# Optimization experiments

Hardware: AMD Instinct MI355X
Metric: run time of the kernel (lower is better)

The kernel has to match this reference:

```python
import jax, jax.numpy as jnp
import numpy as np

B, S, H, E, K, NH = 2, 2048, 1024, 8, 2, 8
HD = H // NH          # head dim = 128
HQ = H // 4           # seasonal encoder width = 256
CAP = int(B * S * 1.5 * K / E)  # expert capacity = 1536


def setup_inputs() -> dict:
    key = jax.random.key(0)
    ks = iter(jax.random.split(key, 32))

    def lin(shape):
        fan_in = shape[0]
        return jax.random.normal(next(ks), shape, jnp.float32) / np.sqrt(fan_in)

    inp = {
        "hidden_states": jax.random.normal(next(ks), (B, S, H), jnp.float32),
        # position embedding table [sequence_length, H]
        "pos_emb": jax.random.normal(next(ks), (S, H), jnp.float32) * 0.02,
        # temporal_encoder: Linear(H+2,H) -> ReLU -> Linear(H,H)
        "We1": lin((H + 2, H)), "be1": jnp.zeros((H,), jnp.float32),
        "We2": lin((H, H)),     "be2": jnp.zeros((H,), jnp.float32),
        # seasonal_encoder: Linear(1,H//4) -> ReLU -> Linear(H//4,H//4)
        "Ws1": lin((1, HQ)),   "bs1": jnp.zeros((HQ,), jnp.float32),
        "Ws2": lin((HQ, HQ)),  "bs2": jnp.zeros((HQ,), jnp.float32),
        # temporal_attention (MultiheadAttention, 8 heads)
        "Wq": lin((H, H)), "bq": jnp.zeros((H,), jnp.float32),
        "Wk": lin((H, H)), "bk": jnp.zeros((H,), jnp.float32),
        "Wv": lin((H, H)), "bv": jnp.zeros((H,), jnp.float32),
        "Wo": lin((H, H)), "bo": jnp.zeros((H,), jnp.float32),
        # temporal_router: Linear(H,H) -> ReLU -> Linear(H,E)
        "Wr1": lin((H, H)), "br1": jnp.zeros((H,), jnp.float32),
        "Wr2": lin((H, E)), "br2": jnp.zeros((E,), jnp.float32),
    }
    return inp


def _forward(hidden_states, pos_emb, We1, be1, We2, be2, Ws1, bs1, Ws2, bs2,
             Wq, bq, Wk, bk, Wv, bv, Wo, bo, Wr1, br1, Wr2, br2):
    b, s, h = hidden_states.shape
    # time features (time_info is None -> defaults)
    t = jnp.arange(s, dtype=jnp.float32)                   # [S]
    season = jnp.sin(t * 2.0 * jnp.pi / 24.0)              # [S]
    time_feat = jnp.broadcast_to(jnp.stack([t, season], -1), (b, s, 2))

    combined = jnp.concatenate([hidden_states, time_feat], axis=-1)  # [B,S,H+2]
    enc = jax.nn.relu(combined @ We1 + be1) @ We2 + be2              # [B,S,H]

    pos = pos_emb[:s]                                                # [S,H]
    seas = jax.nn.relu(season[:, None] @ Ws1 + bs1) @ Ws2 + bs2      # [S,H//4]
    seas_full = jnp.tile(seas, (1, h // seas.shape[-1]))             # [S,H] (expand to H)

    x = enc + pos[None] + seas_full[None]                            # [B,S,H]

    # self-attention (eval mode, no dropout)
    def heads(y):
        return y.reshape(b, s, NH, HD)
    q = heads(x @ Wq + bq)
    k = heads(x @ Wk + bk)
    v = heads(x @ Wv + bv)
    scores = jnp.einsum('bqhd,bkhd->bhqk', q, k) / np.sqrt(HD)
    attn = jax.nn.softmax(scores, axis=-1)
    ctx = jnp.einsum('bhqk,bkhd->bqhd', attn, v).reshape(b, s, h)
    x = ctx @ Wo + bo

    logits = jax.nn.relu(x @ Wr1 + br1) @ Wr2 + br2                  # [B,S,E]
    probs = jax.nn.softmax(logits, axis=-1)

    topv, topi = jax.lax.top_k(probs, K)                             # [B,S,K]
    topv = topv / topv.sum(-1, keepdims=True)

    onehot = jax.nn.one_hot(topi, E, dtype=probs.dtype)              # [B,S,K,E]
    disp0 = onehot.sum(-2)                                           # [B,S,E] (0/1)
    comb0 = (topv[..., None] * onehot).sum(-2)                       # [B,S,E]

    # only capacity slot 0 is ever written (per original code)
    dispatch = jnp.zeros((b, s, E, CAP), probs.dtype).at[..., 0].set(disp0)
    combine = jnp.zeros((b, s, E, CAP), probs.dtype).at[..., 0].set(comb0)

    p_mean = probs.mean(axis=(0, 1))                                 # [E]
    aux_loss = jnp.sum(p_mean * jnp.log(p_mean * E + 1e-9))
    return dispatch, combine, probs, aux_loss


def reference(hidden_states, pos_emb, We1, be1, We2, be2, Ws1, bs1, Ws2, bs2,
              Wq, bq, Wk, bk, Wv, bv, Wo, bo, Wr1, br1, Wr2, br2):
    return _forward(hidden_states, pos_emb, We1, be1, We2, be2, Ws1, bs1, Ws2, bs2,
                    Wq, bq, Wk, bk, Wv, bv, Wo, bo, Wr1, br1, Wr2, br2)
```

## Files before the change

### kernel.cpp

```cpp
#include <hip/hip_runtime.h>
#include <hip/hip_fp16.h>
#include <math.h>

#define N_TOK 4096
#define S_LEN 2048
#define H_DIM 1024
#define E_EXP 8
#define CAPV  1536
#define NHEAD 8
#define HDHD  128

typedef __attribute__((ext_vector_type(8))) _Float16 v8h;
typedef __attribute__((ext_vector_type(4))) float v4f;

__device__ __forceinline__ void splitf16(float v, unsigned short& h, unsigned short& l) {
    __half hh = __float2half(v);
    h = __half_as_ushort(hh);
    l = __half_as_ushort(__float2half(v - __half2float(hh)));
}

__device__ __forceinline__ void gld_lds16(const void* g, void* l) {
    __builtin_amdgcn_global_load_lds(
        (const __attribute__((address_space(1))) unsigned int*)g,
        (__attribute__((address_space(3))) unsigned int*)l,
        16, 0, 0);
}

__global__ __launch_bounds__(256) void prep_k(
    const float* __restrict__ hid, unsigned short* __restrict__ hi,
    unsigned short* __restrict__ lo,
    const float* __restrict__ Ws1, const float* __restrict__ bs1,
    const float* __restrict__ Ws2, const float* __restrict__ bs2,
    float* __restrict__ seasons, float* __restrict__ seas24,
    const float* __restrict__ Wr2, float* __restrict__ wr2t) {
    __shared__ float hbuf[256];
    int blk = blockIdx.x;
    int tid = threadIdx.x;
    if (blk < 4096) {
        int i = blk * 256 + tid;
        float4 v = ((const float4*)hid)[i];
        ushort4 h, l;
        splitf16(v.x, h.x, l.x);
        splitf16(v.y, h.y, l.y);
        splitf16(v.z, h.z, l.z);
        splitf16(v.w, h.w, l.w);
        ((ushort4*)hi)[i] = h;
        ((ushort4*)lo)[i] = l;
    } else if (blk < 4104) {
        int s = (blk - 4096) * 256 + tid;
        if (s < S_LEN) {
            double a = (double)s * 2.0 * M_PI / 24.0;
            seasons[s] = (float)sin(a);
        }
    } else if (blk < 4128) {
        int m = blk - 4104;
        double a = (double)m * 2.0 * M_PI / 24.0;
        float sv = (float)sin(a);
        int j = tid;
        hbuf[j] = fmaxf(sv * Ws1[j] + bs1[j], 0.f);
        __syncthreads();
        float acc = bs2[j];
        for (int i = 0; i < 256; ++i) acc = fmaf(hbuf[i], Ws2[i * 256 + j], acc);
        seas24[m * 256 + j] = acc;
    } else {
        int i = (blk - 4128) * 256 + tid;
        int k = i >> 3, e = i & 7;
        wr2t[e * 1024 + k] = Wr2[i];
    }
}

__device__ __forceinline__ void wconv_body(const float* __restrict__ W,
                                           unsigned short* __restrict__ Thi,
                                           unsigned short* __restrict__ Tlo) {
    __shared__ unsigned short Hs[64][65];
    __shared__ unsigned short Ls[64][65];
    int k0 = blockIdx.y * 64, n0 = blockIdx.x * 64;
    int tid = threadIdx.x;
#pragma unroll
    for (int i = 0; i < 4; ++i) {
        int idx = tid + i * 256;
        int kk = idx >> 4, n4 = idx & 15;
        float4 v = *(const float4*)(W + (size_t)(k0 + kk) * 1024 + n0 + n4 * 4);
        unsigned short h, l;
        splitf16(v.x, h, l); Hs[n4 * 4 + 0][kk] = h; Ls[n4 * 4 + 0][kk] = l;
        splitf16(v.y, h, l); Hs[n4 * 4 + 1][kk] = h; Ls[n4 * 4 + 1][kk] = l;
        splitf16(v.z, h, l); Hs[n4 * 4 + 2][kk] = h; Ls[n4 * 4 + 2][kk] = l;
        splitf16(v.w, h, l); Hs[n4 * 4 + 3][kk] = h; Ls[n4 * 4 + 3][kk] = l;
    }
    __syncthreads();
#pragma unroll
    for (int i = 0; i < 4; ++i) {
        int idx = tid + i * 256;
        int n = idx >> 4, k4 = idx & 15;
        ushort4 h = make_ushort4(Hs[n][k4 * 4], Hs[n][k4 * 4 + 1], Hs[n][k4 * 4 + 2], Hs[n][k4 * 4 + 3]);
        ushort4 l = make_ushort4(Ls[n][k4 * 4], Ls[n][k4 * 4 + 1], Ls[n][k4 * 4 + 2], Ls[n][k4 * 4 + 3]);
        *(ushort4*)(Thi + (size_t)(n0 + n) * 1024 + k0 + k4 * 4) = h;
        *(ushort4*)(Tlo + (size_t)(n0 + n) * 1024 + k0 + k4 * 4) = l;
    }
}

struct WBatch {
    const float* src[7];
    unsigned short* dh[7];
    unsigned short* dl[7];
};

__global__ __launch_bounds__(256) void wconv_batch_k(WBatch wb) {
    int i = blockIdx.z;
    wconv_body(wb.src[i], wb.dh[i], wb.dl[i]);
}

template <int MODE, int EMITF, int EMITS, int EMITT>
__global__ __launch_bounds__(256, 2) void gemm_split(
    const unsigned short* __restrict__ Ahi, const unsigned short* __restrict__ Alo,
    const unsigned short* __restrict__ WThi, const unsigned short* __restrict__ WTlo,
    const float* __restrict__ bias, float* __restrict__ Cf,
    unsigned short* __restrict__ Chi, unsigned short* __restrict__ Clo,
    const float* __restrict__ rowT, const float* __restrict__ rowS,
    const float* __restrict__ seasons, const float* __restrict__ pos,
    const float* __restrict__ seas24, float escale) {
    __shared__ unsigned short Ash[2][128 * 32];
    __shared__ unsigned short Asl[2][128 * 32];
    __shared__ unsigned short Bsh[2][64 * 32];
    __shared__ unsigned short Bsl[2][64 * 32];
    int tid = threadIdx.x;
    int lane = tid & 63, w = tid >> 6;
    int l15 = lane & 15, l16 = lane >> 4;
    int wm = (w >> 1) * 64, wn = (w & 1) * 32;

    int bid = blockIdx.x;
    int mp = (bid & 7) + ((bid >> 7) << 3);
    int np = (bid >> 3) & 15;
    int m0 = mp * 128, n0 = np * 64;

    int ac0 = w * 128 + lane;
    int ac1 = ac0 + 64;
    int bc  = w * 64 + lane;
    int ar0 = ac0 >> 2, ar1 = ac1 >> 2, bn = bc >> 2;
    size_t a_src0 = (size_t)(m0 + ar0) * 1024 + (((ac0 & 3) ^ (ar0 & 3)) * 8);
    size_t a_src1 = (size_t)(m0 + ar1) * 1024 + (((ac1 & 3) ^ (ar1 & 3)) * 8);
    size_t b_src  = (size_t)(n0 + bn) * 1024 + (((bc & 3) ^ (bn & 3)) * 8);

    int a_off[4], b_off[2];
#pragma unroll
    for (int mi = 0; mi < 4; ++mi) {
        int row = wm + mi * 16 + l15;
        a_off[mi] = row * 32 + ((l16 ^ (row & 3)) * 8);
    }
#pragma unroll
    for (int ni = 0; ni < 2; ++ni) {
        int n = wn + ni * 16 + l15;
        b_off[ni] = n * 32 + ((l16 ^ (n & 3)) * 8);
    }

    auto STAGE = [&](int buf, int k0) {
        gld_lds16(Ahi + a_src0 + k0, &Ash[buf][ac0 * 8]);
        gld_lds16(Ahi + a_src1 + k0, &Ash[buf][ac1 * 8]);
        gld_lds16(Alo + a_src0 + k0, &Asl[buf][ac0 * 8]);
        gld_lds16(Alo + a_src1 + k0, &Asl[buf][ac1 * 8]);
        gld_lds16(WThi + b_src + k0, &Bsh[buf][bc * 8]);
        gld_lds16(WTlo + b_src + k0, &Bsl[buf][bc * 8]);
    };

    v4f acc[4][2] = {};
    STAGE(0, 0);
    __syncthreads();

    for (int kk = 0; kk < 32; ++kk) {
        int cur = kk & 1;
        if (kk < 31) STAGE(cur ^ 1, (kk + 1) * 32);
        v8h ah[4], al[4], bh[2], bl[2];
#pragma unroll
        for (int mi = 0; mi < 4; ++mi) {
            ah[mi] = *(const v8h*)&Ash[cur][a_off[mi]];
            al[mi] = *(const v8h*)&Asl[cur][a_off[mi]];
        }
#pragma unroll
        for (int ni = 0; ni < 2; ++ni) {
            bh[ni] = *(const v8h*)&Bsh[cur][b_off[ni]];
            bl[ni] = *(const v8h*)&Bsl[cur][b_off[ni]];
        }
#pragma unroll
        for (int mi = 0; mi < 4; ++mi)
#pragma unroll
            for (int ni = 0; ni < 2; ++ni) {
                acc[mi][ni] = __builtin_amdgcn_mfma_f32_16x16x32_f16(ah[mi], bh[ni], acc[mi][ni], 0, 0, 0);
                acc[mi][ni] = __builtin_amdgcn_mfma_f32_16x16x32_f16(al[mi], bh[ni], acc[mi][ni], 0, 0, 0);
                acc[mi][ni] = __builtin_amdgcn_mfma_f32_16x16x32_f16(ah[mi], bl[ni], acc[mi][ni], 0, 0, 0);
            }
        __syncthreads();
    }

    if (EMITT) {
#pragma unroll
        for (int mi = 0; mi < 4; ++mi) {
            int row0 = m0 + wm + mi * 16 + l16 * 4;
            int bb = row0 >> 11, ss = row0 & 2047;
#pragma unroll
            for (int ni = 0; ni < 2; ++ni) {
                int col = n0 + wn + ni * 16 + l15;
                int hh = col >> 7, dd = col & 127;
                size_t base = ((size_t)((bb * 8 + hh) * 128 + dd)) * 2048 + ss;
                ushort4 vh, vl;
                float v0 = acc[mi][ni][0] + bias[col];
                float v1 = acc[mi][ni][1] + bias[col];
                float v2 = acc[mi][ni][2] + bias[col];
                float v3 = acc[mi][ni][3] + bias[col];
                splitf16(v0, vh.x, vl.x);
                splitf16(v1, vh.y, vl.y);
                splitf16(v2, vh.z, vl.z);
                splitf16(v3, vh.w, vl.w);
                *(ushort4*)(Chi + base) = vh;
                *(ushort4*)(Clo + base) = vl;
            }
        }
    } else {
#pragma unroll
        for (int mi = 0; mi < 4; ++mi) {
#pragma unroll
            for (int r = 0; r < 4; ++r) {
                int row = m0 + wm + mi * 16 + l16 * 4 + r;
                int s = row & (S_LEN - 1);
                float tval = 0.f, seval = 0.f;
                if (MODE == 1) { tval = (float)s; seval = seasons[s]; }
#pragma unroll
                for (int ni = 0; ni < 2; ++ni) {
                    int col = n0 + wn + ni * 16 + l15;
                    float v = acc[mi][ni][r] + bias[col];
                    if (MODE == 1) v += tval * rowT[col] + seval * rowS[col];
                    if (MODE == 2) v += pos[(size_t)s * 1024 + col] + seas24[(s % 24) * 256 + (col & 255)];
                    if (MODE == 1 || MODE == 3) v = fmaxf(v, 0.f);
                    size_t o = (size_t)row * 1024 + col;
                    if (EMITF) Cf[o] = v;
                    if (EMITS) {
                        unsigned short hu, lu;
                        splitf16(v * escale, hu, lu);
                        Chi[o] = hu; Clo[o] = lu;
                    }
                }
            }
        }
    }
}

__global__ __launch_bounds__(256, 2) void gemm_qkv(
    const unsigned short* __restrict__ Ahi, const unsigned short* __restrict__ Alo,
    const unsigned short* __restrict__ WT3hi, const unsigned short* __restrict__ WT3lo,
    const float* __restrict__ bq, const float* __restrict__ bk,
    const float* __restrict__ bv,
    unsigned short* __restrict__ Qhi, unsigned short* __restrict__ Qlo,
    unsigned short* __restrict__ Khi, unsigned short* __restrict__ Klo,
    unsigned short* __restrict__ VThi, unsigned short* __restrict__ VTlo,
    float qscale) {
    __shared__ unsigned short Ash[2][128 * 32];
    __shared__ unsigned short Asl[2][128 * 32];
    __shared__ unsigned short Bsh[2][64 * 32];
    __shared__ unsigned short Bsl[2][64 * 32];
    int tid = threadIdx.x;
    int lane = tid & 63, w = tid >> 6;
    int l15 = lane & 15, l16 = lane >> 4;
    int wm = (w >> 1) * 64, wn = (w & 1) * 32;

    int bid = blockIdx.x;
    int t = bid >> 3;
    int mp = (bid & 7) + (t / 48) * 8;
    int np = t % 48;
    int m0 = mp * 128;
    int wn0 = np * 64;

    int ac0 = w * 128 + lane;
    int ac1 = ac0 + 64;
    int bc  = w * 64 + lane;
    int ar0 = ac0 >> 2, ar1 = ac1 >> 2, bn = bc >> 2;
    size_t a_src0 = (size_t)(m0 + ar0) * 1024 + (((ac0 & 3) ^ (ar0 & 3)) * 8);
    size_t a_src1 = (size_t)(m0 + ar1) * 1024 + (((ac1 & 3) ^ (ar1 & 3)) * 8);
    size_t b_src  = (size_t)(wn0 + bn) * 1024 + (((bc & 3) ^ (bn & 3)) * 8);

    int a_off[4], b_off[2];
#pragma unroll
    for (int mi = 0; mi < 4; ++mi) {
        int row = wm + mi * 16 + l15;
        a_off[mi] = row * 32 + ((l16 ^ (row & 3)) * 8);
    }
#pragma unroll
    for (int ni = 0; ni < 2; ++ni) {
        int n = wn + ni * 16 + l15;
        b_off[ni] = n * 32 + ((l16 ^ (n & 3)) * 8);
    }

    auto STAGE = [&](int buf, int k0) {
        gld_lds16(Ahi + a_src0 + k0, &Ash[buf][ac0 * 8]);
        gld_lds16(Ahi + a_src1 + k0, &Ash[buf][ac1 * 8]);
        gld_lds16(Alo + a_src0 + k0, &Asl[buf][ac0 * 8]);
        gld_lds16(Alo + a_src1 + k0, &Asl[buf][ac1 * 8]);
        gld_lds16(WT3hi + b_src + k0, &Bsh[buf][bc * 8]);
        gld_lds16(WT3lo + b_src + k0, &Bsl[buf][bc * 8]);
    };

    v4f acc[4][2] = {};
    STAGE(0, 0);
    __syncthreads();

    for (int kk = 0; kk < 32; ++kk) {
        int cur = kk & 1;
        if (kk < 31) STAGE(cur ^ 1, (kk + 1) * 32);
        v8h ah[4], al[4], bh[2], bl[2];
#pragma unroll
        for (int mi = 0; mi < 4; ++mi) {
            ah[mi] = *(const v8h*)&Ash[cur][a_off[mi]];
            al[mi] = *(const v8h*)&Asl[cur][a_off[mi]];
        }
#pragma unroll
        for (int ni = 0; ni < 2; ++ni) {
            bh[ni] = *(const v8h*)&Bsh[cur][b_off[ni]];
            bl[ni] = *(const v8h*)&Bsl[cur][b_off[ni]];
        }
#pragma unroll
        for (int mi = 0; mi < 4; ++mi)
#pragma unroll
            for (int ni = 0; ni < 2; ++ni) {
                acc[mi][ni] = __builtin_amdgcn_mfma_f32_16x16x32_f16(ah[mi], bh[ni], acc[mi][ni], 0, 0, 0);
                acc[mi][ni] = __builtin_amdgcn_mfma_f32_16x16x32_f16(al[mi], bh[ni], acc[mi][ni], 0, 0, 0);
                acc[mi][ni] = __builtin_amdgcn_mfma_f32_16x16x32_f16(ah[mi], bl[ni], acc[mi][ni], 0, 0, 0);
            }
        __syncthreads();
    }

    if (np >= 32) {
        const float* bias = bv;
        int n0 = (np - 32) * 64;
#pragma unroll
        for (int mi = 0; mi < 4; ++mi) {
            int row0 = m0 + wm + mi * 16 + l16 * 4;
            int bb = row0 >> 11, ss = row0 & 2047;
#pragma unroll
            for (int ni = 0; ni < 2; ++ni) {
                int col = n0 + wn + ni * 16 + l15;
                int hh = col >> 7, dd = col & 127;
                size_t base = ((size_t)((bb * 8 + hh) * 128 + dd)) * 2048 + ss;
                ushort4 vh, vl;
                float v0 = acc[mi][ni][0] + bias[col];
                float v1 = acc[mi][ni][1] + bias[col];
                float v2 = acc[mi][ni][2] + bias[col];
                float v3 = acc[mi][ni][3] + bias[col];
                splitf16(v0, vh.x, vl.x);
                splitf16(v1, vh.y, vl.y);
                splitf16(v2, vh.z, vl.z);
                splitf16(v3, vh.w, vl.w);
                *(ushort4*)(VThi + base) = vh;
                *(ushort4*)(VTlo + base) = vl;
            }
        }
    } else {
        const float* bias = np < 16 ? bq : bk;
        unsigned short* Dhi = np < 16 ? Qhi : Khi;
        unsigned short* Dlo = np < 16 ? Qlo : Klo;
        float esc = np < 16 ? qscale : 1.f;
        int n0 = (np & 15) * 64;
#pragma unroll
        for (int mi = 0; mi < 4; ++mi) {
#pragma unroll
            for (int r = 0; r < 4; ++r) {
                int row = m0 + wm + mi * 16 + l16 * 4 + r;
#pragma unroll
                for (int ni = 0; ni < 2; ++ni) {
                    int col = n0 + wn + ni * 16 + l15;
                    float v = (acc[mi][ni][r] + bias[col]) * esc;
                    size_t o = (size_t)row * 1024 + col;
                    unsigned short hu, lu;
                    splitf16(v, hu, lu);
                    Dhi[o] = hu; Dlo[o] = lu;
                }
            }
        }
    }
}

__global__ __launch_bounds__(256, 4) void attn_mfma_k(
    const unsigned short* __restrict__ qhi, const unsigned short* __restrict__ qlo,
    const unsigned short* __restrict__ khi, const unsigned short* __restrict__ klo,
    const unsigned short* __restrict__ vthi, const unsigned short* __restrict__ vtlo,
    float* __restrict__ OP, float* __restrict__ ML) {
    __shared__ unsigned short Ks_hi[32 * 128];
    __shared__ unsigned short Ks_lo[32 * 128];
    __shared__ unsigned short Vs_hi[128 * 32];
    __shared__ unsigned short Vs_lo[128 * 32];
    __shared__ unsigned int   Ps[64 * 32];

    int p = blockIdx.x;
    int x = (p >> 3) & 31;
    int g = (p & 7) + ((p >> 8) << 3);
    int bh = g >> 1, z = g & 1;
    int b = bh >> 3, h = bh & 7;
    int q0 = x * 64;
    int tid = threadIdx.x;
    int lane = tid & 63, w = tid >> 6;
    int l15 = lane & 15, l16 = lane >> 4;
    int wm = w * 16;

    v8h qa_h[4], qa_l[4];
    {
        size_t qrow = (size_t)(b * S_LEN + q0 + wm + l15) * H_DIM + h * HDHD;
#pragma unroll
        for (int ks = 0; ks < 4; ++ks) {
            qa_h[ks] = *(const v8h*)(qhi + qrow + ks * 32 + l16 * 8);
            qa_l[ks] = *(const v8h*)(qlo + qrow + ks * 32 + l16 * 8);
        }
    }

    int ktok1 = tid >> 4, kslot1 = tid & 15;
    int ktok2 = ktok1 + 16;
    size_t ksrc1 = (size_t)(b * S_LEN + ktok1) * H_DIM + h * HDHD + ((kslot1 ^ (ktok1 & 7)) * 8);
    size_t ksrc2 = (size_t)(b * S_LEN + ktok2) * H_DIM + h * HDHD + ((kslot1 ^ (ktok2 & 7)) * 8);
    int vd1 = tid >> 2, vslot1 = tid & 3;
    int vd2 = vd1 + 64;
    size_t vsrc1 = (size_t)(bh * HDHD + vd1) * S_LEN + ((vslot1 ^ ((vd1 >> 1) & 3)) * 8);
    size_t vsrc2 = (size_t)(bh * HDHD + vd2) * S_LEN + ((vslot1 ^ ((vd2 >> 1) & 3)) * 8);

    v4f accO[8] = {};
    float mreg[4] = {-1e30f, -1e30f, -1e30f, -1e30f};
    float lreg[4] = {};

    int kt0 = z * 1024;
    for (int it = 0; it < 32; ++it) {
        int kt = kt0 + it * 32;
        __syncthreads();
        size_t koff = (size_t)kt * H_DIM;
        gld_lds16(khi + ksrc1 + koff, &Ks_hi[tid * 8]);
        gld_lds16(khi + ksrc2 + koff, &Ks_hi[(tid + 256) * 8]);
        gld_lds16(klo + ksrc1 + koff, &Ks_lo[tid * 8]);
        gld_lds16(klo + ksrc2 + koff, &Ks_lo[(tid + 256) * 8]);
        gld_lds16(vthi + vsrc1 + kt, &Vs_hi[tid * 8]);
        gld_lds16(vthi + vsrc2 + kt, &Vs_hi[(tid + 256) * 8]);
        gld_lds16(vtlo + vsrc1 + kt, &Vs_lo[tid * 8]);
        gld_lds16(vtlo + vsrc2 + kt, &Vs_lo[(tid + 256) * 8]);
        __syncthreads();

        v4f s0 = {}, s1 = {};
#pragma unroll
        for (int ks = 0; ks < 4; ++ks) {
#pragma unroll
            for (int nt = 0; nt < 2; ++nt) {
                int tok = nt * 16 + l15;
                int slot = (ks * 4 + l16) ^ (tok & 7);
                v8h bhf = *(const v8h*)&Ks_hi[tok * 128 + slot * 8];
                v8h blf = *(const v8h*)&Ks_lo[tok * 128 + slot * 8];
                v4f& ss = nt ? s1 : s0;
                ss = __builtin_amdgcn_mfma_f32_16x16x32_f16(qa_h[ks], bhf, ss, 0, 0, 0);
                ss = __builtin_amdgcn_mfma_f32_16x16x32_f16(qa_l[ks], bhf, ss, 0, 0, 0);
                ss = __builtin_amdgcn_mfma_f32_16x16x32_f16(qa_h[ks], blf, ss, 0, 0, 0);
            }
        }

        float p0[4], p1[4], alpha[4];
#pragma unroll
        for (int r = 0; r < 4; ++r) {
            float tmax = fmaxf(s0[r], s1[r]);
            tmax = fmaxf(tmax, __shfl_xor(tmax, 1));
            tmax = fmaxf(tmax, __shfl_xor(tmax, 2));
            tmax = fmaxf(tmax, __shfl_xor(tmax, 4));
            tmax = fmaxf(tmax, __shfl_xor(tmax, 8));
            float mnew = fmaxf(mreg[r], tmax);
            alpha[r] = __expf(mreg[r] - mnew);
            p0[r] = __expf(s0[r] - mnew);
            p1[r] = __expf(s1[r] - mnew);
            float lt = p0[r] + p1[r];
            lt += __shfl_xor(lt, 1);
            lt += __shfl_xor(lt, 2);
            lt += __shfl_xor(lt, 4);
            lt += __shfl_xor(lt, 8);
            lreg[r] = lreg[r] * alpha[r] + lt;
            mreg[r] = mnew;
        }
#pragma unroll
        for (int nt = 0; nt < 8; ++nt)
#pragma unroll
            for (int r = 0; r < 4; ++r) accO[nt][r] *= alpha[r];

#pragma unroll
        for (int r = 0; r < 4; ++r) {
            int qq = wm + l16 * 4 + r;
            unsigned short ph, pl;
            splitf16(p0[r], ph, pl);
            int k0i = l15;
            Ps[qq * 32 + ((((k0i >> 2) ^ (qq & 7)) << 2) | (k0i & 3))] =
                (unsigned)ph | ((unsigned)pl << 16);
            splitf16(p1[r], ph, pl);
            int k1i = 16 + l15;
            Ps[qq * 32 + ((((k1i >> 2) ^ (qq & 7)) << 2) | (k1i & 3))] =
                (unsigned)ph | ((unsigned)pl << 16);
        }

        int qq = wm + l15;
        int sA = (l16 * 2) ^ (qq & 7);
        int sB = (l16 * 2 + 1) ^ (qq & 7);
        uint4 ua = *(const uint4*)&Ps[qq * 32 + sA * 4];
        uint4 ub = *(const uint4*)&Ps[qq * 32 + sB * 4];
        uint4 ahw, alw;
        ahw.x = (ua.x & 0xffffu) | (ua.y << 16);
        ahw.y = (ua.z & 0xffffu) | (ua.w << 16);
        ahw.z = (ub.x & 0xffffu) | (ub.y << 16);
        ahw.w = (ub.z & 0xffffu) | (ub.w << 16);
        alw.x = (ua.x >> 16) | (ua.y & 0xffff0000u);
        alw.y = (ua.z >> 16) | (ua.w & 0xffff0000u);
        alw.z = (ub.x >> 16) | (ub.y & 0xffff0000u);
        alw.w = (ub.z >> 16) | (ub.w & 0xffff0000u);
        v8h pA_h = __builtin_bit_cast(v8h, ahw);
        v8h pA_l = __builtin_bit_cast(v8h, alw);
#pragma unroll
        for (int nt = 0; nt < 8; ++nt) {
            int d = nt * 16 + l15;
            int slot = l16 ^ ((d >> 1) & 3);
            v8h vhf = *(const v8h*)&Vs_hi[d * 32 + slot * 8];
            v8h vlf = *(const v8h*)&Vs_lo[d * 32 + slot * 8];
            accO[nt] = __builtin_amdgcn_mfma_f32_16x16x32_f16(pA_h, vhf, accO[nt], 0, 0, 0);
            accO[nt] = __builtin_amdgcn_mfma_f32_16x16x32_f16(pA_l, vhf, accO[nt], 0, 0, 0);
            accO[nt] = __builtin_amdgcn_mfma_f32_16x16x32_f16(pA_h, vlf, accO[nt], 0, 0, 0);
        }
    }

#pragma unroll
    for (int r = 0; r < 4; ++r) {
        if (l15 == 0) {
            int q = q0 + wm + l16 * 4 + r;
            size_t mlo = ((size_t)(z * 16 + bh) * 2048 + q) * 2;
            ML[mlo] = mreg[r];
            ML[mlo + 1] = lreg[r];
        }
    }
#pragma unroll
    for (int nt = 0; nt < 8; ++nt) {
#pragma unroll
        for (int r = 0; r < 4; ++r) {
            int q = q0 + wm + l16 * 4 + r;
            size_t o = ((size_t)(z * 16 + bh) * 2048 + q) * 128 + nt * 16 + l15;
            OP[o] = accO[nt][r];
        }
    }
}

__global__ __launch_bounds__(256) void attn_combine_k(
    const float* __restrict__ OP, const float* __restrict__ ML,
    unsigned short* __restrict__ ctx_hi, unsigned short* __restrict__ ctx_lo) {
    int tid = threadIdx.x;
    int R = blockIdx.x * 16 + (tid >> 4);
    int bh = R >> 11, q = R & 2047;
    int b = bh >> 3, h = bh & 7;
    int d0 = (tid & 15) * 8;
    size_t ml0 = ((size_t)bh * 2048 + q) * 2;
    size_t ml1 = ((size_t)(16 + bh) * 2048 + q) * 2;
    float m0 = ML[ml0], l0 = ML[ml0 + 1];
    float m1 = ML[ml1], l1 = ML[ml1 + 1];
    float m = fmaxf(m0, m1);
    float w0 = __expf(m0 - m), w1 = __expf(m1 - m);
    float inv = 1.f / (w0 * l0 + w1 * l1);
    const float* O0 = OP + ((size_t)bh * 2048 + q) * 128 + d0;
    const float* O1 = OP + ((size_t)(16 + bh) * 2048 + q) * 128 + d0;
    size_t dst = ((size_t)(b * 2048 + q)) * 1024 + h * 128 + d0;
    float4 a0 = *(const float4*)O0;
    float4 a1 = *(const float4*)(O0 + 4);
    float4 c0 = *(const float4*)O1;
    float4 c1 = *(const float4*)(O1 + 4);
    ushort4 h0, h1, lo0, lo1;
    splitf16((w0 * a0.x + w1 * c0.x) * inv, h0.x, lo0.x);
    splitf16((w0 * a0.y + w1 * c0.y) * inv, h0.y, lo0.y);
    splitf16((w0 * a0.z + w1 * c0.z) * inv, h0.z, lo0.z);
    splitf16((w0 * a0.w + w1 * c0.w) * inv, h0.w, lo0.w);
    splitf16((w0 * a1.x + w1 * c1.x) * inv, h1.x, lo1.x);
    splitf16((w0 * a1.y + w1 * c1.y) * inv, h1.y, lo1.y);
    splitf16((w0 * a1.z + w1 * c1.z) * inv, h1.z, lo1.z);
    splitf16((w0 * a1.w + w1 * c1.w) * inv, h1.w, lo1.w);
    *(ushort4*)(ctx_hi + dst) = h0;
    *(ushort4*)(ctx_hi + dst + 4) = h1;
    *(ushort4*)(ctx_lo + dst) = lo0;
    *(ushort4*)(ctx_lo + dst + 4) = lo1;
}

__global__ __launch_bounds__(256) void fill_k(float* __restrict__ out) {
    size_t idx = (size_t)blockIdx.x * 256 + threadIdx.x;
    const size_t stride = (size_t)2048 * 256;
    v4f z = {0.f, 0.f, 0.f, 0.f};
    v4f* o = (v4f*)out;
#pragma unroll
    for (int i = 0; i < 48; ++i)
        __builtin_nontemporal_store(z, o + idx + (size_t)i * stride);
}

__global__ __launch_bounds__(256) void logits_k(const float* __restrict__ h1,
                                                const float* __restrict__ Wr2T,
                                                const float* __restrict__ br2,
                                                float* __restrict__ logits) {
    __shared__ float part[256];
    int tid = threadIdx.x;
    int tok8 = tid >> 5;
    int e = (tid >> 2) & 7;
    int ch = tid & 3;
    int tok = blockIdx.x * 8 + tok8;
    const float4* h4 = (const float4*)(h1 + (size_t)tok * 1024 + ch * 256);
    const float4* w4 = (const float4*)(Wr2T + (size_t)e * 1024 + ch * 256);
    float acc = 0.f;
#pragma unroll
    for (int i = 0; i < 64; ++i) {
        float4 a = h4[i];
        float4 bb = w4[i];
        acc = fmaf(a.x, bb.x, fmaf(a.y, bb.y, fmaf(a.z, bb.z, fmaf(a.w, bb.w, acc))));
    }
    part[tid] = acc;
    __syncthreads();
    if (ch == 0) {
        float s = part[tid] + part[tid + 1] + part[tid + 2] + part[tid + 3] + br2[e];
        logits[(size_t)tok * 8 + e] = s;
    }
}

__global__ __launch_bounds__(256) void topk_scatter_k(const float* __restrict__ logits,
                                                      float* __restrict__ out) {
    int tok = blockIdx.x * 256 + threadIdx.x;
    if (tok >= N_TOK) return;
    float l[8], p[8];
    float mx = -1e30f;
#pragma unroll
    for (int e = 0; e < 8; ++e) { l[e] = logits[(size_t)tok * 8 + e]; mx = fmaxf(mx, l[e]); }
    float sum = 0.f;
#pragma unroll
    for (int e = 0; e < 8; ++e) { p[e] = __expf(l[e] - mx); sum += p[e]; }
    float inv = 1.f / sum;
#pragma unroll
    for (int e = 0; e < 8; ++e) p[e] *= inv;
    const size_t NEC = (size_t)N_TOK * E_EXP * CAPV;
    float* probs_out = out + 2 * NEC;
#pragma unroll
    for (int e = 0; e < 8; ++e) probs_out[(size_t)tok * 8 + e] = p[e];
    int i1 = 0;
#pragma unroll
    for (int e = 1; e < 8; ++e) if (p[e] > p[i1]) i1 = e;
    int i2 = -1;
#pragma unroll
    for (int e = 0; e < 8; ++e) {
        if (e == i1) continue;
        if (i2 < 0 || p[e] > p[i2]) i2 = e;
    }
    float v1 = p[i1], v2 = p[i2], tv = v1 + v2;
    size_t base = (size_t)tok * E_EXP * CAPV;
    out[base + (size_t)i1 * CAPV] = 1.f;
    out[base + (size_t)i2 * CAPV] = 1.f;
    out[NEC + base + (size_t)i1 * CAPV] = v1 / tv;
    out[NEC + base + (size_t)i2 * CAPV] = v2 / tv;
}

__global__ void aux_k(const float* __restrict__ probs, float* __restrict__ out_aux) {
    __shared__ float part[256];
    int tid = threadIdx.x;
    int e = tid & 7, chunk = tid >> 3;
    float s = 0.f;
    for (int t = chunk * 128; t < (chunk + 1) * 128; ++t)
        s += probs[(size_t)t * 8 + e];
    part[tid] = s;
    __syncthreads();
    if (tid < 8) {
        float tot = 0.f;
        for (int c = 0; c < 32; ++c) tot += part[c * 8 + e];
        part[tid] = tot / (float)N_TOK;
    }
    __syncthreads();
    if (tid == 0) {
        float aux = 0.f;
        for (int e2 = 0; e2 < 8; ++e2) {
            float pm = part[e2];
            aux += pm * logf(pm * 8.f + 1e-9f);
        }
        *out_aux = aux;
    }
}

extern "C" void kernel_launch(void* const* d_in, const int* in_sizes, int n_in,
                              void* d_out, int out_size, void* d_ws, size_t ws_size,
                              hipStream_t stream) {
    const float* hid = (const float*)d_in[0];
    const float* pos = (const float*)d_in[1];
    const float* We1 = (const float*)d_in[2];
    const float* be1 = (const float*)d_in[3];
    const float* We2 = (const float*)d_in[4];
    const float* be2 = (const float*)d_in[5];
    const float* Ws1 = (const float*)d_in[6];
    const float* bs1 = (const float*)d_in[7];
    const float* Ws2 = (const float*)d_in[8];
    const float* bs2 = (const float*)d_in[9];
    const float* Wq  = (const float*)d_in[10]; const float* bq = (const float*)d_in[11];
    const float* Wk  = (const float*)d_in[12]; const float* bk = (const float*)d_in[13];
    const float* Wv  = (const float*)d_in[14]; const float* bv = (const float*)d_in[15];
    const float* Wo  = (const float*)d_in[16]; const float* bo = (const float*)d_in[17];
    const float* Wr1 = (const float*)d_in[18]; const float* br1 = (const float*)d_in[19];
    const float* Wr2 = (const float*)d_in[20]; const float* br2 = (const float*)d_in[21];

    float* out = (float*)d_out;
    char* base = (char*)d_ws;
    const size_t AC  = (size_t)N_TOK * H_DIM;
    const size_t SPC = AC * 2;
    const size_t FB  = AC * 4;
    const size_t MB  = (size_t)1 << 20;

    unsigned short* B1hi = (unsigned short*)(base);
    unsigned short* B1lo = (unsigned short*)(base + SPC);
    unsigned short* B2hi = (unsigned short*)(base + FB);
    unsigned short* B2lo = (unsigned short*)(base + FB + SPC);
    unsigned short* Qhi  = (unsigned short*)(base + 2 * FB);
    unsigned short* Qlo  = (unsigned short*)(base + 2 * FB + SPC);
    unsigned short* Khi  = (unsigned short*)(base + 3 * FB);
    unsigned short* Klo  = (unsigned short*)(base + 3 * FB + SPC);
    unsigned short* VThi = (unsigned short*)(base + 4 * FB);
    unsigned short* VTlo = (unsigned short*)(base + 4 * FB + SPC);
    float* h1f = (float*)(base + 3 * FB);

    char* wp = base + 5 * FB;
    unsigned short* We1hi = (unsigned short*)(wp);
    unsigned short* We1lo = (unsigned short*)(wp + 2 * MB);
    unsigned short* We2hi = (unsigned short*)(wp + 4 * MB);
    unsigned short* We2lo = (unsigned short*)(wp + 6 * MB);
    unsigned short* QKVhi = (unsigned short*)(wp + 8 * MB);
    unsigned short* QKVlo = (unsigned short*)(wp + 14 * MB);
    unsigned short* Wohi  = (unsigned short*)(wp + 20 * MB);
    unsigned short* Wolo  = (unsigned short*)(wp + 22 * MB);
    unsigned short* Wr1hi = (unsigned short*)(wp + 24 * MB);
    unsigned short* Wr1lo = (unsigned short*)(wp + 26 * MB);
    char* smalls = wp + 28 * MB;
    float* wr2t    = (float*)smalls;
    float* seas24  = wr2t + 8192;
    float* seasons = seas24 + 6144;
    float* logits  = seasons + 2048;

    const size_t NEC = (size_t)N_TOK * E_EXP * CAPV;
    const float QSCALE = 0.08838834764831845f;

    float* OP = out;
    float* ML = out + (size_t)2 * 16 * 2048 * 128;

    dim3 blk(256);

    prep_k<<<4160, 256, 0, stream>>>(hid, B1hi, B1lo, Ws1, bs1, Ws2, bs2,
                                     seasons, seas24, Wr2, wr2t);

    WBatch wb;
    wb.src[0] = We1; wb.dh[0] = We1hi; wb.dl[0] = We1lo;
    wb.src[1] = We2; wb.dh[1] = We2hi; wb.dl[1] = We2lo;
    wb.src[2] = Wq;  wb.dh[2] = QKVhi;                     wb.dl[2] = QKVlo;
    wb.src[3] = Wk;  wb.dh[3] = QKVhi + (size_t)1024 * 1024;  wb.dl[3] = QKVlo + (size_t)1024 * 1024;
    wb.src[4] = Wv;  wb.dh[4] = QKVhi + (size_t)2048 * 1024;  wb.dl[4] = QKVlo + (size_t)2048 * 1024;
    wb.src[5] = Wo;  wb.dh[5] = Wohi;  wb.dl[5] = Wolo;
    wb.src[6] = Wr1; wb.dh[6] = Wr1hi; wb.dl[6] = Wr1lo;
    wconv_batch_k<<<dim3(16, 16, 7), blk, 0, stream>>>(wb);

    gemm_split<1, 0, 1, 0><<<512, blk, 0, stream>>>(B1hi, B1lo, We1hi, We1lo, be1,
        nullptr, B2hi, B2lo,
        We1 + (size_t)1024 * 1024, We1 + (size_t)1025 * 1024, seasons, nullptr, nullptr, 1.f);
    gemm_split<2, 0, 1, 0><<<512, blk, 0, stream>>>(B2hi, B2lo, We2hi, We2lo, be2,
        nullptr, B1hi, B1lo, nullptr, nullptr, nullptr, pos, seas24, 1.f);

    gemm_qkv<<<1536, blk, 0, stream>>>(B1hi, B1lo, QKVhi, QKVlo, bq, bk, bv,
                                       Qhi, Qlo, Khi, Klo, VThi, VTlo, QSCALE);

    attn_mfma_k<<<1024, 256, 0, stream>>>(Qhi, Qlo, Khi, Klo, VThi, VTlo, OP, ML);
    attn_combine_k<<<2048, 256, 0, stream>>>(OP, ML, B2hi, B2lo);

    fill_k<<<2048, 256, 0, stream>>>(out);

    gemm_split<0, 0, 1, 0><<<512, blk, 0, stream>>>(B2hi, B2lo, Wohi, Wolo, bo,
        nullptr, B1hi, B1lo, nullptr, nullptr, nullptr, nullptr, nullptr, 1.f);
    gemm_split<3, 1, 0, 0><<<512, blk, 0, stream>>>(B1hi, B1lo, Wr1hi, Wr1lo, br1,
        h1f, nullptr, nullptr, nullptr, nullptr, nullptr, nullptr, nullptr, 1.f);

    logits_k<<<512, 256, 0, stream>>>(h1f, wr2t, br2, logits);
    topk_scatter_k<<<16, 256, 0, stream>>>(logits, out);
    aux_k<<<1, 256, 0, stream>>>(out + 2 * NEC, out + 2 * NEC + (size_t)N_TOK * E_EXP);
}
```

Measured before the change: 599.3 us.

## Fold output zero-fill into extra blocks of QKV and Wo GEMM launches

New measurement: 565.8 us. -5.6%, faster.

```diff
diff --git a/kernel.cpp b/kernel.cpp
--- a/kernel.cpp
+++ b/kernel.cpp
@@ -9,6 +9,9 @@
 #define CAPV  1536
 #define NHEAD 8
 #define HDHD  128
+
+#define SCRATCH_F4 2129920u
+#define TOTAL_F4   25165824u
 
 typedef __attribute__((ext_vector_type(8))) _Float16 v8h;
 typedef __attribute__((ext_vector_type(4))) float v4f;
@@ -110,7 +113,15 @@
     wconv_body(wb.src[i], wb.dh[i], wb.dl[i]);
 }
 
-template <int MODE, int EMITF, int EMITS, int EMITT>
+__device__ __forceinline__ void fill_body(float* __restrict__ p, size_t f40, size_t f41, int nblk) {
+    v4f z = {0.f, 0.f, 0.f, 0.f};
+    v4f* o = (v4f*)p;
+    size_t n = f41 - f40;
+    for (size_t i = (size_t)blockIdx.x * 256 + threadIdx.x; i < n; i += (size_t)nblk * 256)
+        __builtin_nontemporal_store(z, o + f40 + i);
+}
+
+template <int MODE, int EMITF, int EMITS, int EMITT, int FILLN>
 __global__ __launch_bounds__(256, 2) void gemm_split(
     const unsigned short* __restrict__ Ahi, const unsigned short* __restrict__ Alo,
     const unsigned short* __restrict__ WThi, const unsigned short* __restrict__ WTlo,
@@ -118,7 +129,13 @@
     unsigned short* __restrict__ Chi, unsigned short* __restrict__ Clo,
     const float* __restrict__ rowT, const float* __restrict__ rowS,
     const float* __restrict__ seasons, const float* __restrict__ pos,
-    const float* __restrict__ seas24, float escale) {
+    const float* __restrict__ seas24, float escale, float* __restrict__ fillp) {
+    if (FILLN > 0) {
+        if (blockIdx.x < (unsigned)FILLN) {
+            fill_body(fillp, 0, SCRATCH_F4, FILLN);
+            return;
+        }
+    }
     __shared__ unsigned short Ash[2][128 * 32];
     __shared__ unsigned short Asl[2][128 * 32];
     __shared__ unsigned short Bsh[2][64 * 32];
@@ -128,7 +145,7 @@
     int l15 = lane & 15, l16 = lane >> 4;
     int wm = (w >> 1) * 64, wn = (w & 1) * 32;
 
-    int bid = blockIdx.x;
+    int bid = blockIdx.x - FILLN;
     int mp = (bid & 7) + ((bid >> 7) << 3);
     int np = (bid >> 3) & 15;
     int m0 = mp * 128, n0 = np * 64;
@@ -243,6 +260,7 @@
     }
 }
 
+#define NFILLQ 256
 __global__ __launch_bounds__(256, 2) void gemm_qkv(
     const unsigned short* __restrict__ Ahi, const unsigned short* __restrict__ Alo,
     const unsigned short* __restrict__ WT3hi, const unsigned short* __restrict__ WT3lo,
@@ -251,7 +269,11 @@
     unsigned short* __restrict__ Qhi, unsigned short* __restrict__ Qlo,
     unsigned short* __restrict__ Khi, unsigned short* __restrict__ Klo,
     unsigned short* __restrict__ VThi, unsigned short* __restrict__ VTlo,
-    float qscale) {
+    float qscale, float* __restrict__ fillp) {
+    if (blockIdx.x < NFILLQ) {
+        fill_body(fillp, SCRATCH_F4, TOTAL_F4, NFILLQ);
+        return;
+    }
     __shared__ unsigned short Ash[2][128 * 32];
     __shared__ unsigned short Asl[2][128 * 32];
     __shared__ unsigned short Bsh[2][64 * 32];
@@ -261,7 +283,7 @@
     int l15 = lane & 15, l16 = lane >> 4;
     int wm = (w >> 1) * 64, wn = (w & 1) * 32;
 
-    int bid = blockIdx.x;
+    int bid = blockIdx.x - NFILLQ;
     int t = bid >> 3;
     int mp = (bid & 7) + (t / 48) * 8;
     int np = t % 48;
@@ -576,16 +598,6 @@
     *(ushort4*)(ctx_lo + dst + 4) = lo1;
 }
 
-__global__ __launch_bounds__(256) void fill_k(float* __restrict__ out) {
-    size_t idx = (size_t)blockIdx.x * 256 + threadIdx.x;
-    const size_t stride = (size_t)2048 * 256;
-    v4f z = {0.f, 0.f, 0.f, 0.f};
-    v4f* o = (v4f*)out;
-#pragma unroll
-    for (int i = 0; i < 48; ++i)
-        __builtin_nontemporal_store(z, o + idx + (size_t)i * stride);
-}
-
 __global__ __launch_bounds__(256) void logits_k(const float* __restrict__ h1,
                                                 const float* __restrict__ Wr2T,
                                                 const float* __restrict__ br2,
@@ -743,31 +755,29 @@
     WBatch wb;
     wb.src[0] = We1; wb.dh[0] = We1hi; wb.dl[0] = We1lo;
     wb.src[1] = We2; wb.dh[1] = We2hi; wb.dl[1] = We2lo;
-    wb.src[2] = Wq;  wb.dh[2] = QKVhi;                     wb.dl[2] = QKVlo;
+    wb.src[2] = Wq;  wb.dh[2] = QKVhi;                        wb.dl[2] = QKVlo;
     wb.src[3] = Wk;  wb.dh[3] = QKVhi + (size_t)1024 * 1024;  wb.dl[3] = QKVlo + (size_t)1024 * 1024;
     wb.src[4] = Wv;  wb.dh[4] = QKVhi + (size_t)2048 * 1024;  wb.dl[4] = QKVlo + (size_t)2048 * 1024;
     wb.src[5] = Wo;  wb.dh[5] = Wohi;  wb.dl[5] = Wolo;
     wb.src[6] = Wr1; wb.dh[6] = Wr1hi; wb.dl[6] = Wr1lo;
     wconv_batch_k<<<dim3(16, 16, 7), blk, 0, stream>>>(wb);
 
-    gemm_split<1, 0, 1, 0><<<512, blk, 0, stream>>>(B1hi, B1lo, We1hi, We1lo, be1,
+    gemm_split<1, 0, 1, 0, 0><<<512, blk, 0, stream>>>(B1hi, B1lo, We1hi, We1lo, be1,
         nullptr, B2hi, B2lo,
-        We1 + (size_t)1024 * 1024, We1 + (size_t)1025 * 1024, seasons, nullptr, nullptr, 1.f);
-    gemm_split<2, 0, 1, 0><<<512, blk, 0, stream>>>(B2hi, B2lo, We2hi, We2lo, be2,
-        nullptr, B1hi, B1lo, nullptr, nullptr, nullptr, pos, seas24, 1.f);
-
-    gemm_qkv<<<1536, blk, 0, stream>>>(B1hi, B1lo, QKVhi, QKVlo, bq, bk, bv,
-                                       Qhi, Qlo, Khi, Klo, VThi, VTlo, QSCALE);
+        We1 + (size_t)1024 * 1024, We1 + (size_t)1025 * 1024, seasons, nullptr, nullptr, 1.f, nullptr);
+    gemm_split<2, 0, 1, 0, 0><<<512, blk, 0, stream>>>(B2hi, B2lo, We2hi, We2lo, be2,
+        nullptr, B1hi, B1lo, nullptr, nullptr, nullptr, pos, seas24, 1.f, nullptr);
+
+    gemm_qkv<<<1536 + NFILLQ, blk, 0, stream>>>(B1hi, B1lo, QKVhi, QKVlo, bq, bk, bv,
+                                                Qhi, Qlo, Khi, Klo, VThi, VTlo, QSCALE, out);
 
     attn_mfma_k<<<1024, 256, 0, stream>>>(Qhi, Qlo, Khi, Klo, VThi, VTlo, OP, ML);
     attn_combine_k<<<2048, 256, 0, stream>>>(OP, ML, B2hi, B2lo);
 
-    fill_k<<<2048, 256, 0, stream>>>(out);
-
-    gemm_split<0, 0, 1, 0><<<512, blk, 0, stream>>>(B2hi, B2lo, Wohi, Wolo, bo,
-        nullptr, B1hi, B1lo, nullptr, nullptr, nullptr, nullptr, nullptr, 1.f);
-    gemm_split<3, 1, 0, 0><<<512, blk, 0, stream>>>(B1hi, B1lo, Wr1hi, Wr1lo, br1,
-        h1f, nullptr, nullptr, nullptr, nullptr, nullptr, nullptr, nullptr, 1.f);
+    gemm_split<0, 0, 1, 0, 64><<<512 + 64, blk, 0, stream>>>(B2hi, B2lo, Wohi, Wolo, bo,
+        nullptr, B1hi, B1lo, nullptr, nullptr, nullptr, nullptr, nullptr, 1.f, out);
+    gemm_split<3, 1, 0, 0, 0><<<512, blk, 0, stream>>>(B1hi, B1lo, Wr1hi, Wr1lo, br1,
+        h1f, nullptr, nullptr, nullptr, nullptr, nullptr, nullptr, nullptr, 1.f, nullptr);
 
     logits_k<<<512, 256, 0, stream>>>(h1f, wr2t, br2, logits);
     topk_scatter_k<<<16, 256, 0, stream>>>(logits, out);
```
